# Optimization experiments

Measured on AMD Instinct MI355X. Metric: run time of the kernel, lower is better.

The kernel has to match this reference:

```python
import jax, jax.numpy as jnp
import numpy as np

# dims
B, T = 128, 1024
INP, HUMAN = 54, 64          # input_dim, output_dim (HUMAN_SIZE)
DEC, ENC = 256, 256          # decoder / encoder GRU sizes
K, H_PSI, LR_PSI = 16, 256, 32
N_PSI = DEC*DEC + DEC + DEC*INP + DEC*HUMAN + INP*(HUMAN-INP)  # 96540


def setup_inputs() -> dict:
    key = jax.random.key(0)
    ks = jax.random.split(key, 16)
    g = lambda i, shape, s=0.05: jax.random.normal(ks[i], shape, jnp.float32) * s
    return {
        "inputs": g(0, (B, T, INP), 1.0),
        "state": jnp.zeros((B, DEC), jnp.float32),
        "eps": g(1, (B, K), 1.0),
        # encoder GRUCell params (torch gate order r,z,n)
        "enc_Wih": g(2, (3*ENC, INP)),
        "enc_Whh": g(3, (3*ENC, ENC)),
        "enc_bih": jnp.zeros((3*ENC,), jnp.float32),
        "enc_bhh": jnp.zeros((3*ENC,), jnp.float32),
        # latent projections
        "to_mu": g(4, (K, ENC)),
        "to_lsigma": g(5, (K, ENC)),
        # psi hypernetwork MLP
        "W1": g(6, (H_PSI, K)),   "b1": jnp.zeros((H_PSI,), jnp.float32),
        "W2": g(7, (LR_PSI, H_PSI)), "b2": jnp.zeros((LR_PSI,), jnp.float32),
        "W3": g(8, (N_PSI, LR_PSI), 0.01), "b3": jnp.zeros((N_PSI,), jnp.float32),
        # shared decoder gate params (bias second half init to ones, as in module)
        "gru_Wih": g(9, (2*DEC, INP)),
        "gru_Whh": g(10, (DEC, 2*DEC)),
        "gru_bias": jnp.concatenate([jnp.zeros((DEC,)), jnp.ones((DEC,))]).astype(jnp.float32),
    }


def reference(inputs, state, eps, enc_Wih, enc_Whh, enc_bih, enc_bhh,
              to_mu, to_lsigma, W1, b1, W2, b2, W3, b3,
              gru_Wih, gru_Whh, gru_bias):
    x_tbd = jnp.swapaxes(inputs, 0, 1)  # [T,B,INP]

    # ---- encoder GRU scan (torch GRUCell semantics) ----
    def enc_step(h, x_t):
        gi = x_t @ enc_Wih.T + enc_bih
        gh = h @ enc_Whh.T + enc_bhh
        ir, iz, inn = jnp.split(gi, 3, axis=-1)
        hr, hz, hn = jnp.split(gh, 3, axis=-1)
        r = jax.nn.sigmoid(ir + hr)
        z = jax.nn.sigmoid(iz + hz)
        n = jnp.tanh(inn + r * hn)
        return (1 - z) * n + z * h, None

    h_enc, _ = jax.lax.scan(enc_step, jnp.zeros((inputs.shape[0], ENC), inputs.dtype), x_tbd)

    # ---- MT latent ----
    mu = h_enc @ to_mu.T                 # [B,K]
    logstd = h_enc @ to_lsigma.T         # [B,K]
    z_lat = mu + eps * jnp.exp(logstd)

    # ---- psi hypernetwork ----
    psi = jnp.tanh(z_lat @ W1.T + b1) @ W2.T + b2
    psi = psi @ W3.T + b3                # [B, N_PSI]

    o = 0
    Whh_p = psi[:, o:o+DEC*DEC].reshape(-1, DEC, DEC); o += DEC*DEC
    bh_p  = psi[:, o:o+DEC];                           o += DEC
    Wih_p = psi[:, o:o+DEC*INP].reshape(-1, DEC, INP); o += DEC*INP
    C_p   = psi[:, o:o+DEC*HUMAN].reshape(-1, DEC, HUMAN); o += DEC*HUMAN
    D_p   = psi[:, o:o+INP*(HUMAN-INP)].reshape(-1, INP, HUMAN-INP)

    # ---- per-sample hypernet-weighted GRU decoder, vectorized over batch ----
    def dec_step(h, x_t):  # h:[B,DEC], x_t:[B,INP]
        gx = x_t @ gru_Wih.T                       # [B,2*DEC]
        gh = h @ gru_Whh                           # [B,2*DEC]
        zt = jax.nn.sigmoid(gx[:, :DEC] + gh[:, :DEC] + gru_bias[:DEC])
        rt = jax.nn.sigmoid(gx[:, DEC:] + gh[:, DEC:] + gru_bias[DEC:])
        eta = jnp.tanh(jnp.einsum('bd,bhd->bh', x_t, Wih_p)
                       + rt * jnp.tanh(jnp.einsum('bh,bhg->bg', h, Whh_p) + bh_p))
        h_new = zt * h + (1 - zt) * eta
        return h_new, h_new

    h_last, dec_seq = jax.lax.scan(dec_step, state, x_tbd)
    dec_seq = jnp.swapaxes(dec_seq, 0, 1)          # [B,T,DEC]

    # yhat = dec@C + cat(zeros, x@D) ; residual adds inputs to first INP cols
    yD = jnp.einsum('btd,bde->bte', inputs, D_p)   # [B,T,HUMAN-INP]
    yhats = jnp.einsum('bth,bho->bto', dec_seq, C_p) + jnp.concatenate([inputs, yD], axis=-1)

    return yhats, mu, logstd, h_last
```

## Files before the change

kernel.cpp:

```cpp
#include <hip/hip_runtime.h>

#define BB 128
#define TT 1024
#define INP 54
#define HUM 64
#define NPSI 96540
#define OFF_BH 65536
#define OFF_WIH 65792
#define OFF_C 79616
#define OFF_D 96000
#define OUT_MU 8388608
#define OUT_LS 8390656
#define OUT_HL 8392704

typedef unsigned int u32;
typedef unsigned short u16;
typedef _Float16 h2 __attribute__((ext_vector_type(2)));

__device__ __forceinline__ u32 pk(float a, float b) {
    h2 v; v.x = (_Float16)a; v.y = (_Float16)b;
    return __builtin_bit_cast(u32, v);
}
__device__ __forceinline__ float f16tof(u16 v) {
    return (float)__builtin_bit_cast(_Float16, v);
}
__device__ __forceinline__ u16 ftof16(float v) {
    return __builtin_bit_cast(u16, (_Float16)v);
}
__device__ __forceinline__ float lo16f(u32 v) { return f16tof((u16)(v & 0xffffu)); }
__device__ __forceinline__ float hi16f(u32 v) { return f16tof((u16)(v >> 16)); }
__device__ __forceinline__ h2 bch2(u32 a) { return __builtin_bit_cast(h2, a); }
__device__ __forceinline__ float fd2(u32 a, u32 b, float c) {
#if __has_builtin(__builtin_amdgcn_fdot2)
    return __builtin_amdgcn_fdot2(bch2(a), bch2(b), c, false);
#else
    return c + lo16f(a) * lo16f(b) + hi16f(a) * hi16f(b);
#endif
}
__device__ __forceinline__ h2 pfma(u32 a, u32 b, h2 c) {
    return bch2(a) * bch2(b) + c;
}
__device__ __forceinline__ float h2tof(h2 s) { return (float)s.x + (float)s.y; }
__device__ __forceinline__ float fsig(float x) { return 1.f / (1.f + __expf(-x)); }
__device__ __forceinline__ float ftanh(float x) { float e = __expf(2.f * x); return 1.f - 2.f / (e + 1.f); }

__device__ __forceinline__ float qred(float v) {
#if __has_builtin(__builtin_amdgcn_mov_dpp)
    int x = __builtin_bit_cast(int, v);
    v += __builtin_bit_cast(float, __builtin_amdgcn_mov_dpp(x, 0xB1, 0xF, 0xF, true));
    x = __builtin_bit_cast(int, v);
    v += __builtin_bit_cast(float, __builtin_amdgcn_mov_dpp(x, 0x4E, 0xF, 0xF, true));
    return v;
#else
    v += __shfl_xor(v, 1); v += __shfl_xor(v, 2);
    return v;
#endif
}

__global__ __launch_bounds__(768, 3) void gemm_x_kernel(
    const float* __restrict__ inp, const float* __restrict__ W0,
    const u16* __restrict__ psi16, int mode, int t0, int len, int ct, int nt,
    u16* __restrict__ gout)
{
    const int tid = threadIdx.x;
    const int b = blockIdx.x / nt, tc = blockIdx.x % nt;
    const int gr = tid;
    float w[INP];
    if (mode == 0 || gr < 512) {
        const float* wsrc = W0 + (size_t)gr * INP;
#pragma unroll
        for (int c = 0; c < INP; ++c) w[c] = wsrc[c];
    } else {
        const u16* wsrc = psi16 + (size_t)b * NPSI + OFF_WIH + (size_t)(gr - 512) * INP;
#pragma unroll
        for (int c = 0; c < INP; ++c) w[c] = f16tof(wsrc[c]);
    }
    const int tb = tc * 128;
    const int te = (tb + 128 < len) ? tb + 128 : len;
    for (int tl = tb; tl < te; ++tl) {
        const float* xr = inp + ((size_t)b * TT + t0 + tl) * INP;
        float a = 0.f;
#pragma unroll
        for (int c = 0; c < INP; ++c) a = __builtin_fmaf(xr[c], w[c], a);
        gout[((size_t)b * ct + tl) * 768 + gr] = ftof16(a);
    }
}

__global__ __launch_bounds__(512) __attribute__((amdgpu_waves_per_eu(2, 2)))
void enc_scan_kernel(
    const u16* __restrict__ gi, int t0, int len, int ct,
    const float* __restrict__ Whh, const float* __restrict__ bih,
    const float* __restrict__ bhh, float* __restrict__ hcarry)
{
    __shared__ __align__(16) u32 hpp[2][144];
    __shared__ __align__(16) u32 gxs[2][3072];
    const int tid = threadIdx.x, b = blockIdx.x;
    const int l = tid & 3, g = tid >> 2;
    const int j0 = 2 * g, j1 = 2 * g + 1;

    u32 wr0[32], wz0[32], wn0[32], wr1[32], wz1[32], wn1[32];
    {
        const float* pr0 = Whh + (size_t)j0 * 256 + 64 * l;
        const float* pz0 = Whh + (size_t)(256 + j0) * 256 + 64 * l;
        const float* pn0 = Whh + (size_t)(512 + j0) * 256 + 64 * l;
        const float* pr1 = Whh + (size_t)j1 * 256 + 64 * l;
        const float* pz1 = Whh + (size_t)(256 + j1) * 256 + 64 * l;
        const float* pn1 = Whh + (size_t)(512 + j1) * 256 + 64 * l;
#pragma unroll
        for (int c = 0; c < 32; ++c) {
            wr0[c] = pk(pr0[2 * c], pr0[2 * c + 1]);
            wz0[c] = pk(pz0[2 * c], pz0[2 * c + 1]);
            wn0[c] = pk(pn0[2 * c], pn0[2 * c + 1]);
            wr1[c] = pk(pr1[2 * c], pr1[2 * c + 1]);
            wz1[c] = pk(pz1[2 * c], pz1[2 * c + 1]);
            wn1[c] = pk(pn1[2 * c], pn1[2 * c + 1]);
        }
    }
    const float brb0 = bih[j0] + bhh[j0],             brb1 = bih[j1] + bhh[j1];
    const float bzb0 = bih[256 + j0] + bhh[256 + j0], bzb1 = bih[256 + j1] + bhh[256 + j1];
    const float bib0 = bih[512 + j0],                 bib1 = bih[512 + j1];
    const float bhb0 = bhh[512 + j0],                 bhb1 = bhh[512 + j1];
    float hc0 = 0.f, hc1 = 0.f;
    if (t0 > 0) { hc0 = hcarry[(size_t)b * 256 + j0]; hc1 = hcarry[(size_t)b * 256 + j1]; }
    if (tid < 128) {
        u32 hv = 0u;
        if (t0 > 0) hv = pk(hcarry[(size_t)b * 256 + 2 * tid], hcarry[(size_t)b * 256 + 2 * tid + 1]);
        hpp[0][36 * (tid >> 5) + (tid & 31)] = hv;
    }
    const u32* gb32 = (const u32*)(gi + (size_t)b * ct * 768);
    {
        const int steps0 = (len < 8) ? len : 8;
#pragma unroll
        for (int k = 0; k < 6; ++k) {
            const int f = k * 512 + tid;
            if (f < 384 * steps0) gxs[0][f] = gb32[f];
        }
    }
    __syncthreads();

    const h2 z2 = {(_Float16)0.f, (_Float16)0.f};
    int buf = 0;
    for (int cb = 0; cb < len; cb += 8) {
        const int steps = (len - cb < 8) ? (len - cb) : 8;
        const int nsteps = (len - cb - 8 < 8) ? (len - cb - 8) : 8;
        u32 stg[6];
        if (nsteps > 0) {
            const u32* gsrc = gb32 + (size_t)(cb + 8) * 384;
#pragma unroll
            for (int k = 0; k < 6; ++k) {
                const int f = k * 512 + tid;
                if (f < 384 * nsteps) stg[k] = gsrc[f];
            }
        }
        for (int st = 0; st < steps; ++st) {
            const int tl = cb + st;
            const int p = tl & 1;
            const u32 c0 = gxs[buf][st * 384 + g];
            const u32 c1 = gxs[buf][st * 384 + 128 + g];
            const u32 c2 = gxs[buf][st * 384 + 256 + g];
            h2 vr0a = z2, vr0b = z2, vz0a = z2, vz0b = z2, vn0a = z2, vn0b = z2;
            h2 vr1a = z2, vr1b = z2, vz1a = z2, vz1b = z2, vn1a = z2, vn1b = z2;
            const uint4* hq = (const uint4*)hpp[p];
#pragma unroll
            for (int cc = 0; cc < 8; ++cc) {
                uint4 q = hq[9 * l + cc];
                u32 qa[4] = {q.x, q.y, q.z, q.w};
#pragma unroll
                for (int u = 0; u < 4; ++u) {
                    const int c = cc * 4 + u;
                    if (u & 1) {
                        vr0b = pfma(wr0[c], qa[u], vr0b);
                        vz0b = pfma(wz0[c], qa[u], vz0b);
                        vn0b = pfma(wn0[c], qa[u], vn0b);
                        vr1b = pfma(wr1[c], qa[u], vr1b);
                        vz1b = pfma(wz1[c], qa[u], vz1b);
                        vn1b = pfma(wn1[c], qa[u], vn1b);
                    } else {
                        vr0a = pfma(wr0[c], qa[u], vr0a);
                        vz0a = pfma(wz0[c], qa[u], vz0a);
                        vn0a = pfma(wn0[c], qa[u], vn0a);
                        vr1a = pfma(wr1[c], qa[u], vr1a);
                        vz1a = pfma(wz1[c], qa[u], vz1a);
                        vn1a = pfma(wn1[c], qa[u], vn1a);
                    }
                }
            }
            float ar0 = qred(h2tof(vr0a + vr0b));
            float az0 = qred(h2tof(vz0a + vz0b));
            float ah0 = qred(h2tof(vn0a + vn0b));
            float ar1 = qred(h2tof(vr1a + vr1b));
            float az1 = qred(h2tof(vz1a + vz1b));
            float ah1 = qred(h2tof(vn1a + vn1b));
            {
                float r0 = fsig(ar0 + lo16f(c0) + brb0);
                float z0 = fsig(az0 + lo16f(c1) + bzb0);
                float nn0 = ftanh(lo16f(c2) + bib0 + r0 * (ah0 + bhb0));
                float hn0 = (1.f - z0) * nn0 + z0 * hc0;
                float r1 = fsig(ar1 + hi16f(c0) + brb1);
                float z1 = fsig(az1 + hi16f(c1) + bzb1);
                float nn1 = ftanh(hi16f(c2) + bib1 + r1 * (ah1 + bhb1));
                float hn1 = (1.f - z1) * nn1 + z1 * hc1;
                hc0 = hn0; hc1 = hn1;
                if (l == 0) hpp[p ^ 1][36 * (g >> 5) + (g & 31)] = pk(hn0, hn1);
            }
            __syncthreads();
        }
        if (nsteps > 0) {
#pragma unroll
            for (int k = 0; k < 6; ++k) {
                const int f = k * 512 + tid;
                if (f < 384 * nsteps) gxs[buf ^ 1][f] = stg[k];
            }
        }
        __syncthreads();
        buf ^= 1;
    }
    if (l == 0) {
        hcarry[(size_t)b * 256 + j0] = hc0;
        hcarry[(size_t)b * 256 + j1] = hc1;
    }
}

__global__ __launch_bounds__(256) void latent_kernel(
    const float* __restrict__ henc, const float* __restrict__ eps,
    const float* __restrict__ to_mu, const float* __restrict__ to_ls,
    const float* __restrict__ W1, const float* __restrict__ b1,
    const float* __restrict__ W2, const float* __restrict__ b2,
    float* __restrict__ psi2, float* __restrict__ out)
{
    __shared__ float h[256], zz[16], p1[256];
    const int tid = threadIdx.x, b = blockIdx.x;
    h[tid] = henc[(size_t)b * 256 + tid];
    __syncthreads();
    if (tid < 16) {
        float m = 0, s = 0;
        for (int k = 0; k < 256; ++k) {
            m += h[k] * to_mu[tid * 256 + k];
            s += h[k] * to_ls[tid * 256 + k];
        }
        out[OUT_MU + b * 16 + tid] = m;
        out[OUT_LS + b * 16 + tid] = s;
        zz[tid] = m + eps[b * 16 + tid] * __expf(s);
    }
    __syncthreads();
    {
        float a = b1[tid];
        for (int k = 0; k < 16; ++k) a += zz[k] * W1[tid * 16 + k];
        p1[tid] = ftanh(a);
    }
    __syncthreads();
    if (tid < 32) {
        float a = b2[tid];
        for (int k = 0; k < 256; ++k) a += p1[k] * W2[tid * 256 + k];
        psi2[b * 32 + tid] = a;
    }
}

__global__ __launch_bounds__(256) void psi3_kernel(
    const float* __restrict__ psi2, const float* __restrict__ W3,
    const float* __restrict__ b3, u16* __restrict__ psi16)
{
    __shared__ float sp2[128 * 32];
    __shared__ float w3t[256 * 33];
    const int tid = threadIdx.x;
    const int n0 = blockIdx.x * 256;
    for (int idx = tid; idx < 4096; idx += 256) sp2[idx] = psi2[idx];
    for (int idx = tid; idx < 8192; idx += 256) {
        int row = idx >> 5, k = idx & 31;
        int n = n0 + row;
        w3t[row * 33 + k] = (n < NPSI) ? W3[(size_t)n * 32 + k] : 0.f;
    }
    __syncthreads();
    const int n = n0 + tid;
    if (n < NPSI) {
        float w[32];
#pragma unroll
        for (int k = 0; k < 32; ++k) w[k] = w3t[tid * 33 + k];
        const float bv = b3[n];
        for (int bi = 0; bi < 128; ++bi) {
            float a = bv;
#pragma unroll
            for (int k = 0; k < 32; ++k) a += sp2[bi * 32 + k] * w[k];
            psi16[(size_t)bi * NPSI + n] = ftof16(a);
        }
    }
}

__global__ __launch_bounds__(512) __attribute__((amdgpu_waves_per_eu(2, 2)))
void dec_scan_kernel(
    const u16* __restrict__ gx, int t0, int len, int ct,
    const float* __restrict__ state, const float* __restrict__ gWhh,
    const float* __restrict__ gbias, const u16* __restrict__ psi16,
    float* __restrict__ dcarry, u32* __restrict__ hseq, float* __restrict__ out)
{
    __shared__ __align__(16) u32 hpp[2][144];
    __shared__ __align__(16) u32 gxs[2][3072];
    const int tid = threadIdx.x, b = blockIdx.x;
    const int l = tid & 3, g = tid >> 2;
    const int j0 = 2 * g, j1 = 2 * g + 1;
    const u16* pc = psi16 + (size_t)b * NPSI;

    u32 wz0[32], wr0[32], wp0[32], wz1[32], wr1[32], wp1[32];
#pragma unroll
    for (int c = 0; c < 32; ++c) {
        const int h0 = 64 * l + 2 * c;
        wz0[c] = pk(gWhh[(size_t)h0 * 512 + j0], gWhh[(size_t)(h0 + 1) * 512 + j0]);
        wr0[c] = pk(gWhh[(size_t)h0 * 512 + 256 + j0], gWhh[(size_t)(h0 + 1) * 512 + 256 + j0]);
        wp0[c] = (u32)pc[(size_t)h0 * 256 + j0] | ((u32)pc[(size_t)(h0 + 1) * 256 + j0] << 16);
        wz1[c] = pk(gWhh[(size_t)h0 * 512 + j1], gWhh[(size_t)(h0 + 1) * 512 + j1]);
        wr1[c] = pk(gWhh[(size_t)h0 * 512 + 256 + j1], gWhh[(size_t)(h0 + 1) * 512 + 256 + j1]);
        wp1[c] = (u32)pc[(size_t)h0 * 256 + j1] | ((u32)pc[(size_t)(h0 + 1) * 256 + j1] << 16);
    }
    const float gzb0 = gbias[j0], gzb1 = gbias[j1];
    const float grb0 = gbias[256 + j0], grb1 = gbias[256 + j1];
    const float bhb0 = f16tof(pc[OFF_BH + j0]), bhb1 = f16tof(pc[OFF_BH + j1]);
    const float* hsrc = (t0 == 0) ? state : dcarry;
    float hc0 = hsrc[(size_t)b * 256 + j0];
    float hc1 = hsrc[(size_t)b * 256 + j1];
    if (tid < 128) hpp[0][36 * (tid >> 5) + (tid & 31)] =
        pk(hsrc[(size_t)b * 256 + 2 * tid], hsrc[(size_t)b * 256 + 2 * tid + 1]);
    const u32* gb32 = (const u32*)(gx + (size_t)b * ct * 768);
    {
        const int steps0 = (len < 8) ? len : 8;
#pragma unroll
        for (int k = 0; k < 6; ++k) {
            const int f = k * 512 + tid;
            if (f < 384 * steps0) gxs[0][f] = gb32[f];
        }
    }
    __syncthreads();

    u32* hsb = hseq + (size_t)b * TT * 128;
    int buf = 0;
    for (int cb = 0; cb < len; cb += 8) {
        const int steps = (len - cb < 8) ? (len - cb) : 8;
        const int nsteps = (len - cb - 8 < 8) ? (len - cb - 8) : 8;
        u32 stg[6];
        if (nsteps > 0) {
            const u32* gsrc = gb32 + (size_t)(cb + 8) * 384;
#pragma unroll
            for (int k = 0; k < 6; ++k) {
                const int f = k * 512 + tid;
                if (f < 384 * nsteps) stg[k] = gsrc[f];
            }
        }
        for (int st = 0; st < steps; ++st) {
            const int tl = cb + st;
            const int p = tl & 1;
            const u32 c0 = gxs[buf][st * 384 + g];
            const u32 c1 = gxs[buf][st * 384 + 128 + g];
            const u32 c2 = gxs[buf][st * 384 + 256 + g];
            float az0 = 0, ar0 = 0, ap0 = 0, az1 = 0, ar1 = 0, ap1 = 0;
            const uint4* hq = (const uint4*)hpp[p];
#pragma unroll
            for (int cc = 0; cc < 8; ++cc) {
                uint4 q = hq[9 * l + cc];
                u32 qa[4] = {q.x, q.y, q.z, q.w};
#pragma unroll
                for (int u = 0; u < 4; ++u) {
                    const int c = cc * 4 + u;
                    az0 = fd2(wz0[c], qa[u], az0);
                    ar0 = fd2(wr0[c], qa[u], ar0);
                    ap0 = fd2(wp0[c], qa[u], ap0);
                    az1 = fd2(wz1[c], qa[u], az1);
                    ar1 = fd2(wr1[c], qa[u], ar1);
                    ap1 = fd2(wp1[c], qa[u], ap1);
                }
            }
            az0 = qred(az0); ar0 = qred(ar0); ap0 = qred(ap0);
            az1 = qred(az1); ar1 = qred(ar1); ap1 = qred(ap1);
            {
                float zt0 = fsig(az0 + lo16f(c0) + gzb0);
                float rt0 = fsig(ar0 + lo16f(c1) + grb0);
                float eta0 = ftanh(lo16f(c2) + rt0 * ftanh(ap0 + bhb0));
                float hn0 = zt0 * hc0 + (1.f - zt0) * eta0;
                float zt1 = fsig(az1 + hi16f(c0) + gzb1);
                float rt1 = fsig(ar1 + hi16f(c1) + grb1);
                float eta1 = ftanh(hi16f(c2) + rt1 * ftanh(ap1 + bhb1));
                float hn1 = zt1 * hc1 + (1.f - zt1) * eta1;
                hc0 = hn0; hc1 = hn1;
                if (l == 0) {
                    u32 hv = pk(hn0, hn1);
                    hpp[p ^ 1][36 * (g >> 5) + (g & 31)] = hv;
                    hsb[(size_t)(t0 + tl) * 128 + g] = hv;
                }
            }
            __syncthreads();
        }
        if (nsteps > 0) {
#pragma unroll
            for (int k = 0; k < 6; ++k) {
                const int f = k * 512 + tid;
                if (f < 384 * nsteps) gxs[buf ^ 1][f] = stg[k];
            }
        }
        __syncthreads();
        buf ^= 1;
    }
    if (l == 0) {
        dcarry[(size_t)b * 256 + j0] = hc0;
        dcarry[(size_t)b * 256 + j1] = hc1;
        if (t0 + len == TT) {
            out[OUT_HL + (size_t)b * 256 + j0] = hc0;
            out[OUT_HL + (size_t)b * 256 + j1] = hc1;
        }
    }
}

#define YT 32
__global__ __launch_bounds__(256) void yhat_kernel(
    const u32* __restrict__ hseq, const u16* __restrict__ psi16,
    float* __restrict__ out)
{
    __shared__ float part[2][YT][64];
    const int tid = threadIdx.x;
    const int b = blockIdx.x >> 5, tile = blockIdx.x & 31;
    const int o = tid & 63, s = (tid >> 6) & 1, tq = tid >> 7;
    const u16* pc = psi16 + (size_t)b * NPSI;
    u32 cpr[64];
#pragma unroll
    for (int i = 0; i < 64; ++i) {
        const int gp = s * 64 + i;
        cpr[i] = (u32)pc[OFF_C + (size_t)(2 * gp) * 64 + o]
               | ((u32)pc[OFF_C + (size_t)(2 * gp + 1) * 64 + o] << 16);
    }
    const int t0 = tile * YT;
    for (int th = 0; th < YT / 2; ++th) {
        const int tl = tq * (YT / 2) + th;
        const uint4* h4 = (const uint4*)(hseq + ((size_t)b * TT + t0 + tl) * 128 + s * 64);
        float a = 0.f;
#pragma unroll
        for (int gc = 0; gc < 16; ++gc) {
            uint4 q = h4[gc];
            a = fd2(q.x, cpr[gc * 4 + 0], a);
            a = fd2(q.y, cpr[gc * 4 + 1], a);
            a = fd2(q.z, cpr[gc * 4 + 2], a);
            a = fd2(q.w, cpr[gc * 4 + 3], a);
        }
        part[s][tl][o] = a;
    }
    __syncthreads();
    for (int i = 0; i < 8; ++i) {
        const int flat = i * 256 + tid;
        const int tl = flat >> 6, o2 = flat & 63;
        out[((size_t)b * TT + t0 + tl) * HUM + o2] = part[0][tl][o2] + part[1][tl][o2];
    }
}

__global__ __launch_bounds__(256) void post_kernel(
    const float* __restrict__ inp, const u16* __restrict__ psi16,
    float* __restrict__ out)
{
    __shared__ float xs[128][55];
    __shared__ float ds[INP][10];
    const int tid = threadIdx.x;
    const int b = blockIdx.x >> 3, tile = blockIdx.x & 7;
    const int t0 = tile * 128;
    const u16* pc = psi16 + (size_t)b * NPSI;
    for (int idx = tid; idx < 540; idx += 256)
        ds[idx / 10][idx % 10] = f16tof(pc[OFF_D + idx]);
    for (int idx = tid; idx < 128 * INP; idx += 256) {
        const int t = idx / INP, d = idx % INP;
        xs[t][d] = inp[((size_t)b * TT + t0 + t) * INP + d];
    }
    __syncthreads();
    for (int i = 0; i < 32; ++i) {
        const int flat = i * 256 + tid;
        const int t = flat >> 6, o = flat & 63;
        const size_t oi = ((size_t)b * TT + t0 + t) * HUM + o;
        float y = out[oi];
        if (o < INP) y += xs[t][o];
        else {
            float acc = 0.f;
            for (int d = 0; d < INP; ++d) acc += xs[t][d] * ds[d][o - INP];
            y += acc;
        }
        out[oi] = y;
    }
}

extern "C" void kernel_launch(void* const* d_in, const int* in_sizes, int n_in,
                              void* d_out, int out_size, void* d_ws, size_t ws_size,
                              hipStream_t stream)
{
    const float* inputs = (const float*)d_in[0];
    const float* state  = (const float*)d_in[1];
    const float* eps    = (const float*)d_in[2];
    const float* eWih   = (const float*)d_in[3];
    const float* eWhh   = (const float*)d_in[4];
    const float* ebih   = (const float*)d_in[5];
    const float* ebhh   = (const float*)d_in[6];
    const float* to_mu  = (const float*)d_in[7];
    const float* to_ls  = (const float*)d_in[8];
    const float* W1     = (const float*)d_in[9];
    const float* b1     = (const float*)d_in[10];
    const float* W2     = (const float*)d_in[11];
    const float* b2     = (const float*)d_in[12];
    const float* W3     = (const float*)d_in[13];
    const float* b3     = (const float*)d_in[14];
    const float* gWih   = (const float*)d_in[15];
    const float* gWhh   = (const float*)d_in[16];
    const float* gbias  = (const float*)d_in[17];
    float* out = (float*)d_out;
    float* ws  = (float*)d_ws;

    float* henc   = ws;
    float* psi2   = ws + 32768;
    float* dcarry = ws + 36864;
    u16*   psi16  = (u16*)(ws + 69632);
    u32*   hseq   = (u32*)(ws + 6248192);
    u16*   gbuf   = (u16*)(ws + 23025408);
    const size_t used = (size_t)23025408 * 4;
    size_t avail = (ws_size > used + 4096) ? (ws_size - used - 4096) : 0;
    int ct = (int)(avail / ((size_t)BB * 768 * 2));
    if (ct > TT) ct = TT;
    if (ct < 1) ct = 1;

    for (int t0 = 0; t0 < TT; t0 += ct) {
        const int len = (TT - t0 < ct) ? (TT - t0) : ct;
        const int nt = (len + 127) / 128;
        gemm_x_kernel<<<BB * nt, 768, 0, stream>>>(inputs, eWih, psi16, 0, t0, len, ct, nt, gbuf);
        enc_scan_kernel<<<BB, 512, 0, stream>>>(gbuf, t0, len, ct, eWhh, ebih, ebhh, henc);
    }
    latent_kernel<<<BB, 256, 0, stream>>>(henc, eps, to_mu, to_ls, W1, b1, W2, b2, psi2, out);
    psi3_kernel<<<(NPSI + 255) / 256, 256, 0, stream>>>(psi2, W3, b3, psi16);
    for (int t0 = 0; t0 < TT; t0 += ct) {
        const int len = (TT - t0 < ct) ? (TT - t0) : ct;
        const int nt = (len + 127) / 128;
        gemm_x_kernel<<<BB * nt, 768, 0, stream>>>(inputs, gWih, psi16, 1, t0, len, ct, nt, gbuf);
        dec_scan_kernel<<<BB, 512, 0, stream>>>(gbuf, t0, len, ct, state, gWhh, gbias, psi16,
                                                dcarry, hseq, out);
    }
    yhat_kernel<<<BB * 32, 256, 0, stream>>>(hseq, psi16, out);
    post_kernel<<<BB * 8, 256, 0, stream>>>(inputs, psi16, out);
}
```

Before: 4.706 ms.

## Split scan kernels to one hidden unit per thread group with 1024 threads

```diff
diff --git a/kernel.cpp b/kernel.cpp
--- a/kernel.cpp
+++ b/kernel.cpp
@@ -37,10 +37,6 @@
     return c + lo16f(a) * lo16f(b) + hi16f(a) * hi16f(b);
 #endif
 }
-__device__ __forceinline__ h2 pfma(u32 a, u32 b, h2 c) {
-    return bch2(a) * bch2(b) + c;
-}
-__device__ __forceinline__ float h2tof(h2 s) { return (float)s.x + (float)s.y; }
 __device__ __forceinline__ float fsig(float x) { return 1.f / (1.f + __expf(-x)); }
 __device__ __forceinline__ float ftanh(float x) { float e = __expf(2.f * x); return 1.f - 2.f / (e + 1.f); }
 
@@ -86,42 +82,35 @@
     }
 }
 
-__global__ __launch_bounds__(512) __attribute__((amdgpu_waves_per_eu(2, 2)))
+__global__ __launch_bounds__(1024) __attribute__((amdgpu_waves_per_eu(4, 4)))
 void enc_scan_kernel(
     const u16* __restrict__ gi, int t0, int len, int ct,
     const float* __restrict__ Whh, const float* __restrict__ bih,
     const float* __restrict__ bhh, float* __restrict__ hcarry)
 {
     __shared__ __align__(16) u32 hpp[2][144];
-    __shared__ __align__(16) u32 gxs[2][3072];
+    __shared__ __align__(16) u32 gxs32[2][3072];
     const int tid = threadIdx.x, b = blockIdx.x;
     const int l = tid & 3, g = tid >> 2;
-    const int j0 = 2 * g, j1 = 2 * g + 1;
-
-    u32 wr0[32], wz0[32], wn0[32], wr1[32], wz1[32], wn1[32];
+
+    u32 wr[32], wz[32], wn[32];
     {
-        const float* pr0 = Whh + (size_t)j0 * 256 + 64 * l;
-        const float* pz0 = Whh + (size_t)(256 + j0) * 256 + 64 * l;
-        const float* pn0 = Whh + (size_t)(512 + j0) * 256 + 64 * l;
-        const float* pr1 = Whh + (size_t)j1 * 256 + 64 * l;
-        const float* pz1 = Whh + (size_t)(256 + j1) * 256 + 64 * l;
-        const float* pn1 = Whh + (size_t)(512 + j1) * 256 + 64 * l;
+        const float* pr = Whh + (size_t)g * 256 + 64 * l;
+        const float* pz = Whh + (size_t)(256 + g) * 256 + 64 * l;
+        const float* pn = Whh + (size_t)(512 + g) * 256 + 64 * l;
 #pragma unroll
         for (int c = 0; c < 32; ++c) {
-            wr0[c] = pk(pr0[2 * c], pr0[2 * c + 1]);
-            wz0[c] = pk(pz0[2 * c], pz0[2 * c + 1]);
-            wn0[c] = pk(pn0[2 * c], pn0[2 * c + 1]);
-            wr1[c] = pk(pr1[2 * c], pr1[2 * c + 1]);
-            wz1[c] = pk(pz1[2 * c], pz1[2 * c + 1]);
-            wn1[c] = pk(pn1[2 * c], pn1[2 * c + 1]);
-        }
-    }
-    const float brb0 = bih[j0] + bhh[j0],             brb1 = bih[j1] + bhh[j1];
-    const float bzb0 = bih[256 + j0] + bhh[256 + j0], bzb1 = bih[256 + j1] + bhh[256 + j1];
-    const float bib0 = bih[512 + j0],                 bib1 = bih[512 + j1];
-    const float bhb0 = bhh[512 + j0],                 bhb1 = bhh[512 + j1];
-    float hc0 = 0.f, hc1 = 0.f;
-    if (t0 > 0) { hc0 = hcarry[(size_t)b * 256 + j0]; hc1 = hcarry[(size_t)b * 256 + j1]; }
+            wr[c] = pk(pr[2 * c], pr[2 * c + 1]);
+            wz[c] = pk(pz[2 * c], pz[2 * c + 1]);
+            wn[c] = pk(pn[2 * c], pn[2 * c + 1]);
+        }
+    }
+    const float brb = bih[g] + bhh[g];
+    const float bzb = bih[256 + g] + bhh[256 + g];
+    const float bib = bih[512 + g];
+    const float bhb = bhh[512 + g];
+    float hc = 0.f;
+    if (t0 > 0) hc = hcarry[(size_t)b * 256 + g];
     if (tid < 128) {
         u32 hv = 0u;
         if (t0 > 0) hv = pk(hcarry[(size_t)b * 256 + 2 * tid], hcarry[(size_t)b * 256 + 2 * tid + 1]);
@@ -131,35 +120,30 @@
     {
         const int steps0 = (len < 8) ? len : 8;
 #pragma unroll
-        for (int k = 0; k < 6; ++k) {
-            const int f = k * 512 + tid;
-            if (f < 384 * steps0) gxs[0][f] = gb32[f];
-        }
-    }
-    __syncthreads();
-
-    const h2 z2 = {(_Float16)0.f, (_Float16)0.f};
+        for (int k = 0; k < 3; ++k) {
+            const int f = k * 1024 + tid;
+            if (f < 384 * steps0) gxs32[0][f] = gb32[f];
+        }
+    }
+    __syncthreads();
+
     int buf = 0;
     for (int cb = 0; cb < len; cb += 8) {
         const int steps = (len - cb < 8) ? (len - cb) : 8;
         const int nsteps = (len - cb - 8 < 8) ? (len - cb - 8) : 8;
-        u32 stg[6];
+        u32 stg[3];
         if (nsteps > 0) {
             const u32* gsrc = gb32 + (size_t)(cb + 8) * 384;
 #pragma unroll
-            for (int k = 0; k < 6; ++k) {
-                const int f = k * 512 + tid;
+            for (int k = 0; k < 3; ++k) {
+                const int f = k * 1024 + tid;
                 if (f < 384 * nsteps) stg[k] = gsrc[f];
             }
         }
         for (int st = 0; st < steps; ++st) {
             const int tl = cb + st;
             const int p = tl & 1;
-            const u32 c0 = gxs[buf][st * 384 + g];
-            const u32 c1 = gxs[buf][st * 384 + 128 + g];
-            const u32 c2 = gxs[buf][st * 384 + 256 + g];
-            h2 vr0a = z2, vr0b = z2, vz0a = z2, vz0b = z2, vn0a = z2, vn0b = z2;
-            h2 vr1a = z2, vr1b = z2, vz1a = z2, vz1b = z2, vn1a = z2, vn1b = z2;
+            float ar = 0, az = 0, ah = 0;
             const uint4* hq = (const uint4*)hpp[p];
 #pragma unroll
             for (int cc = 0; cc < 8; ++cc) {
@@ -168,57 +152,41 @@
 #pragma unroll
                 for (int u = 0; u < 4; ++u) {
                     const int c = cc * 4 + u;
-                    if (u & 1) {
-                        vr0b = pfma(wr0[c], qa[u], vr0b);
-                        vz0b = pfma(wz0[c], qa[u], vz0b);
-                        vn0b = pfma(wn0[c], qa[u], vn0b);
-                        vr1b = pfma(wr1[c], qa[u], vr1b);
-                        vz1b = pfma(wz1[c], qa[u], vz1b);
-                        vn1b = pfma(wn1[c], qa[u], vn1b);
-                    } else {
-                        vr0a = pfma(wr0[c], qa[u], vr0a);
-                        vz0a = pfma(wz0[c], qa[u], vz0a);
-                        vn0a = pfma(wn0[c], qa[u], vn0a);
-                        vr1a = pfma(wr1[c], qa[u], vr1a);
-                        vz1a = pfma(wz1[c], qa[u], vz1a);
-                        vn1a = pfma(wn1[c], qa[u], vn1a);
-                    }
+                    ar = fd2(wr[c], qa[u], ar);
+                    az = fd2(wz[c], qa[u], az);
+                    ah = fd2(wn[c], qa[u], ah);
                 }
             }
-            float ar0 = qred(h2tof(vr0a + vr0b));
-            float az0 = qred(h2tof(vz0a + vz0b));
-            float ah0 = qred(h2tof(vn0a + vn0b));
-            float ar1 = qred(h2tof(vr1a + vr1b));
-            float az1 = qred(h2tof(vz1a + vz1b));
-            float ah1 = qred(h2tof(vn1a + vn1b));
-            {
-                float r0 = fsig(ar0 + lo16f(c0) + brb0);
-                float z0 = fsig(az0 + lo16f(c1) + bzb0);
-                float nn0 = ftanh(lo16f(c2) + bib0 + r0 * (ah0 + bhb0));
-                float hn0 = (1.f - z0) * nn0 + z0 * hc0;
-                float r1 = fsig(ar1 + hi16f(c0) + brb1);
-                float z1 = fsig(az1 + hi16f(c1) + bzb1);
-                float nn1 = ftanh(hi16f(c2) + bib1 + r1 * (ah1 + bhb1));
-                float hn1 = (1.f - z1) * nn1 + z1 * hc1;
-                hc0 = hn0; hc1 = hn1;
-                if (l == 0) hpp[p ^ 1][36 * (g >> 5) + (g & 31)] = pk(hn0, hn1);
+            ar = qred(ar); az = qred(az); ah = qred(ah);
+            if (l == 0) {
+                const u16* gx16 = (const u16*)gxs32[buf];
+                const float c0 = f16tof(gx16[st * 768 + g]);
+                const float c1 = f16tof(gx16[st * 768 + 256 + g]);
+                const float c2 = f16tof(gx16[st * 768 + 512 + g]);
+                float r = fsig(ar + c0 + brb);
+                float z = fsig(az + c1 + bzb);
+                float nn = ftanh(c2 + bib + r * (ah + bhb));
+                float hn = (1.f - z) * nn + z * hc;
+                hc = hn;
+                float ho = __shfl_xor(hn, 4);
+                if (!(g & 1)) {
+                    const int gp = g >> 1;
+                    hpp[p ^ 1][36 * (gp >> 5) + (gp & 31)] = pk(hn, ho);
+                }
             }
             __syncthreads();
         }
         if (nsteps > 0) {
 #pragma unroll
-            for (int k = 0; k < 6; ++k) {
-                const int f = k * 512 + tid;
-                if (f < 384 * nsteps) gxs[buf ^ 1][f] = stg[k];
+            for (int k = 0; k < 3; ++k) {
+                const int f = k * 1024 + tid;
+                if (f < 384 * nsteps) gxs32[buf ^ 1][f] = stg[k];
             }
         }
         __syncthreads();
         buf ^= 1;
     }
-    if (l == 0) {
-        hcarry[(size_t)b * 256 + j0] = hc0;
-        hcarry[(size_t)b * 256 + j1] = hc1;
-    }
+    if (l == 0) hcarry[(size_t)b * 256 + g] = hc;
 }
 
 __global__ __launch_bounds__(256) void latent_kernel(
@@ -286,7 +254,7 @@
     }
 }
 
-__global__ __launch_bounds__(512) __attribute__((amdgpu_waves_per_eu(2, 2)))
+__global__ __launch_bounds__(1024) __attribute__((amdgpu_waves_per_eu(4, 4)))
 void dec_scan_kernel(
     const u16* __restrict__ gx, int t0, int len, int ct,
     const float* __restrict__ state, const float* __restrict__ gWhh,
@@ -294,38 +262,33 @@
     float* __restrict__ dcarry, u32* __restrict__ hseq, float* __restrict__ out)
 {
     __shared__ __align__(16) u32 hpp[2][144];
-    __shared__ __align__(16) u32 gxs[2][3072];
+    __shared__ __align__(16) u32 gxs32[2][3072];
     const int tid = threadIdx.x, b = blockIdx.x;
     const int l = tid & 3, g = tid >> 2;
-    const int j0 = 2 * g, j1 = 2 * g + 1;
     const u16* pc = psi16 + (size_t)b * NPSI;
 
-    u32 wz0[32], wr0[32], wp0[32], wz1[32], wr1[32], wp1[32];
+    u32 wz[32], wrr[32], wp[32];
 #pragma unroll
     for (int c = 0; c < 32; ++c) {
         const int h0 = 64 * l + 2 * c;
-        wz0[c] = pk(gWhh[(size_t)h0 * 512 + j0], gWhh[(size_t)(h0 + 1) * 512 + j0]);
-        wr0[c] = pk(gWhh[(size_t)h0 * 512 + 256 + j0], gWhh[(size_t)(h0 + 1) * 512 + 256 + j0]);
-        wp0[c] = (u32)pc[(size_t)h0 * 256 + j0] | ((u32)pc[(size_t)(h0 + 1) * 256 + j0] << 16);
-        wz1[c] = pk(gWhh[(size_t)h0 * 512 + j1], gWhh[(size_t)(h0 + 1) * 512 + j1]);
-        wr1[c] = pk(gWhh[(size_t)h0 * 512 + 256 + j1], gWhh[(size_t)(h0 + 1) * 512 + 256 + j1]);
-        wp1[c] = (u32)pc[(size_t)h0 * 256 + j1] | ((u32)pc[(size_t)(h0 + 1) * 256 + j1] << 16);
-    }
-    const float gzb0 = gbias[j0], gzb1 = gbias[j1];
-    const float grb0 = gbias[256 + j0], grb1 = gbias[256 + j1];
-    const float bhb0 = f16tof(pc[OFF_BH + j0]), bhb1 = f16tof(pc[OFF_BH + j1]);
+        wz[c]  = pk(gWhh[(size_t)h0 * 512 + g], gWhh[(size_t)(h0 + 1) * 512 + g]);
+        wrr[c] = pk(gWhh[(size_t)h0 * 512 + 256 + g], gWhh[(size_t)(h0 + 1) * 512 + 256 + g]);
+        wp[c]  = (u32)pc[(size_t)h0 * 256 + g] | ((u32)pc[(size_t)(h0 + 1) * 256 + g] << 16);
+    }
+    const float gzb = gbias[g];
+    const float grb = gbias[256 + g];
+    const float bhb = f16tof(pc[OFF_BH + g]);
     const float* hsrc = (t0 == 0) ? state : dcarry;
-    float hc0 = hsrc[(size_t)b * 256 + j0];
-    float hc1 = hsrc[(size_t)b * 256 + j1];
+    float hc = hsrc[(size_t)b * 256 + g];
     if (tid < 128) hpp[0][36 * (tid >> 5) + (tid & 31)] =
         pk(hsrc[(size_t)b * 256 + 2 * tid], hsrc[(size_t)b * 256 + 2 * tid + 1]);
     const u32* gb32 = (const u32*)(gx + (size_t)b * ct * 768);
     {
         const int steps0 = (len < 8) ? len : 8;
 #pragma unroll
-        for (int k = 0; k < 6; ++k) {
-            const int f = k * 512 + tid;
-            if (f < 384 * steps0) gxs[0][f] = gb32[f];
+        for (int k = 0; k < 3; ++k) {
+            const int f = k * 1024 + tid;
+            if (f < 384 * steps0) gxs32[0][f] = gb32[f];
         }
     }
     __syncthreads();
@@ -335,22 +298,19 @@
     for (int cb = 0; cb < len; cb += 8) {
         const int steps = (len - cb < 8) ? (len - cb) : 8;
         const int nsteps = (len - cb - 8 < 8) ? (len - cb - 8) : 8;
-        u32 stg[6];
+        u32 stg[3];
         if (nsteps > 0) {
             const u32* gsrc = gb32 + (size_t)(cb + 8) * 384;
 #pragma unroll
-            for (int k = 0; k < 6; ++k) {
-                const int f = k * 512 + tid;
+            for (int k = 0; k < 3; ++k) {
+                const int f = k * 1024 + tid;
                 if (f < 384 * nsteps) stg[k] = gsrc[f];
             }
         }
         for (int st = 0; st < steps; ++st) {
             const int tl = cb + st;
             const int p = tl & 1;
-            const u32 c0 = gxs[buf][st * 384 + g];
-            const u32 c1 = gxs[buf][st * 384 + 128 + g];
-            const u32 c2 = gxs[buf][st * 384 + 256 + g];
-            float az0 = 0, ar0 = 0, ap0 = 0, az1 = 0, ar1 = 0, ap1 = 0;
+            float az = 0, ar = 0, ap = 0;
             const uint4* hq = (const uint4*)hpp[p];
 #pragma unroll
             for (int cc = 0; cc < 8; ++cc) {
@@ -359,51 +319,45 @@
 #pragma unroll
                 for (int u = 0; u < 4; ++u) {
                     const int c = cc * 4 + u;
-                    az0 = fd2(wz0[c], qa[u], az0);
-                    ar0 = fd2(wr0[c], qa[u], ar0);
-                    ap0 = fd2(wp0[c], qa[u], ap0);
-                    az1 = fd2(wz1[c], qa[u], az1);
-                    ar1 = fd2(wr1[c], qa[u], ar1);
-                    ap1 = fd2(wp1[c], qa[u], ap1);
+                    az = fd2(wz[c], qa[u], az);
+                    ar = fd2(wrr[c], qa[u], ar);
+                    ap = fd2(wp[c], qa[u], ap);
                 }
             }
-            az0 = qred(az0); ar0 = qred(ar0); ap0 = qred(ap0);
-            az1 = qred(az1); ar1 = qred(ar1); ap1 = qred(ap1);
-            {
-                float zt0 = fsig(az0 + lo16f(c0) + gzb0);
-                float rt0 = fsig(ar0 + lo16f(c1) + grb0);
-                float eta0 = ftanh(lo16f(c2) + rt0 * ftanh(ap0 + bhb0));
-                float hn0 = zt0 * hc0 + (1.f - zt0) * eta0;
-                float zt1 = fsig(az1 + hi16f(c0) + gzb1);
-                float rt1 = fsig(ar1 + hi16f(c1) + grb1);
-                float eta1 = ftanh(hi16f(c2) + rt1 * ftanh(ap1 + bhb1));
-                float hn1 = zt1 * hc1 + (1.f - zt1) * eta1;
-                hc0 = hn0; hc1 = hn1;
-                if (l == 0) {
-                    u32 hv = pk(hn0, hn1);
-                    hpp[p ^ 1][36 * (g >> 5) + (g & 31)] = hv;
-                    hsb[(size_t)(t0 + tl) * 128 + g] = hv;
+            az = qred(az); ar = qred(ar); ap = qred(ap);
+            if (l == 0) {
+                const u16* gx16 = (const u16*)gxs32[buf];
+                const float c0 = f16tof(gx16[st * 768 + g]);
+                const float c1 = f16tof(gx16[st * 768 + 256 + g]);
+                const float c2 = f16tof(gx16[st * 768 + 512 + g]);
+                float zt = fsig(az + c0 + gzb);
+                float rt = fsig(ar + c1 + grb);
+                float eta = ftanh(c2 + rt * ftanh(ap + bhb));
+                float hn = zt * hc + (1.f - zt) * eta;
+                hc = hn;
+                float ho = __shfl_xor(hn, 4);
+                if (!(g & 1)) {
+                    const int gp = g >> 1;
+                    u32 hv = pk(hn, ho);
+                    hpp[p ^ 1][36 * (gp >> 5) + (gp & 31)] = hv;
+                    hsb[(size_t)(t0 + tl) * 128 + gp] = hv;
                 }
             }
             __syncthreads();
         }
         if (nsteps > 0) {
 #pragma unroll
-            for (int k = 0; k < 6; ++k) {
-                const int f = k * 512 + tid;
-                if (f < 384 * nsteps) gxs[buf ^ 1][f] = stg[k];
+            for (int k = 0; k < 3; ++k) {
+                const int f = k * 1024 + tid;
+                if (f < 384 * nsteps) gxs32[buf ^ 1][f] = stg[k];
             }
         }
         __syncthreads();
         buf ^= 1;
     }
     if (l == 0) {
-        dcarry[(size_t)b * 256 + j0] = hc0;
-        dcarry[(size_t)b * 256 + j1] = hc1;
-        if (t0 + len == TT) {
-            out[OUT_HL + (size_t)b * 256 + j0] = hc0;
-            out[OUT_HL + (size_t)b * 256 + j1] = hc1;
-        }
+        dcarry[(size_t)b * 256 + g] = hc;
+        if (t0 + len == TT) out[OUT_HL + (size_t)b * 256 + g] = hc;
     }
 }
 
@@ -520,7 +474,7 @@
         const int len = (TT - t0 < ct) ? (TT - t0) : ct;
         const int nt = (len + 127) / 128;
         gemm_x_kernel<<<BB * nt, 768, 0, stream>>>(inputs, eWih, psi16, 0, t0, len, ct, nt, gbuf);
-        enc_scan_kernel<<<BB, 512, 0, stream>>>(gbuf, t0, len, ct, eWhh, ebih, ebhh, henc);
+        enc_scan_kernel<<<BB, 1024, 0, stream>>>(gbuf, t0, len, ct, eWhh, ebih, ebhh, henc);
     }
     latent_kernel<<<BB, 256, 0, stream>>>(henc, eps, to_mu, to_ls, W1, b1, W2, b2, psi2, out);
     psi3_kernel<<<(NPSI + 255) / 256, 256, 0, stream>>>(psi2, W3, b3, psi16);
@@ -528,8 +482,8 @@
         const int len = (TT - t0 < ct) ? (TT - t0) : ct;
         const int nt = (len + 127) / 128;
         gemm_x_kernel<<<BB * nt, 768, 0, stream>>>(inputs, gWih, psi16, 1, t0, len, ct, nt, gbuf);
-        dec_scan_kernel<<<BB, 512, 0, stream>>>(gbuf, t0, len, ct, state, gWhh, gbias, psi16,
-                                                dcarry, hseq, out);
+        dec_scan_kernel<<<BB, 1024, 0, stream>>>(gbuf, t0, len, ct, state, gWhh, gbias, psi16,
+                                                 dcarry, hseq, out);
     }
     yhat_kernel<<<BB * 32, 256, 0, stream>>>(hseq, psi16, out);
     post_kernel<<<BB * 8, 256, 0, stream>>>(inputs, psi16, out);
```

After: 5.173 ms. 1.1x slower.

## Simplify encoder scan: per-step register prefetch of gates and fp32 dot2 accumulation

Applied to the files above, without the earlier changes.

```diff
diff --git a/kernel.cpp b/kernel.cpp
--- a/kernel.cpp
+++ b/kernel.cpp
@@ -37,10 +37,6 @@
     return c + lo16f(a) * lo16f(b) + hi16f(a) * hi16f(b);
 #endif
 }
-__device__ __forceinline__ h2 pfma(u32 a, u32 b, h2 c) {
-    return bch2(a) * bch2(b) + c;
-}
-__device__ __forceinline__ float h2tof(h2 s) { return (float)s.x + (float)s.y; }
 __device__ __forceinline__ float fsig(float x) { return 1.f / (1.f + __expf(-x)); }
 __device__ __forceinline__ float ftanh(float x) { float e = __expf(2.f * x); return 1.f - 2.f / (e + 1.f); }
 
@@ -93,7 +89,6 @@
     const float* __restrict__ bhh, float* __restrict__ hcarry)
 {
     __shared__ __align__(16) u32 hpp[2][144];
-    __shared__ __align__(16) u32 gxs[2][3072];
     const int tid = threadIdx.x, b = blockIdx.x;
     const int l = tid & 3, g = tid >> 2;
     const int j0 = 2 * g, j1 = 2 * g + 1;
@@ -127,93 +122,55 @@
         if (t0 > 0) hv = pk(hcarry[(size_t)b * 256 + 2 * tid], hcarry[(size_t)b * 256 + 2 * tid + 1]);
         hpp[0][36 * (tid >> 5) + (tid & 31)] = hv;
     }
-    const u32* gb32 = (const u32*)(gi + (size_t)b * ct * 768);
-    {
-        const int steps0 = (len < 8) ? len : 8;
-#pragma unroll
-        for (int k = 0; k < 6; ++k) {
-            const int f = k * 512 + tid;
-            if (f < 384 * steps0) gxs[0][f] = gb32[f];
-        }
-    }
-    __syncthreads();
-
-    const h2 z2 = {(_Float16)0.f, (_Float16)0.f};
-    int buf = 0;
-    for (int cb = 0; cb < len; cb += 8) {
-        const int steps = (len - cb < 8) ? (len - cb) : 8;
-        const int nsteps = (len - cb - 8 < 8) ? (len - cb - 8) : 8;
-        u32 stg[6];
-        if (nsteps > 0) {
-            const u32* gsrc = gb32 + (size_t)(cb + 8) * 384;
-#pragma unroll
-            for (int k = 0; k < 6; ++k) {
-                const int f = k * 512 + tid;
-                if (f < 384 * nsteps) stg[k] = gsrc[f];
+    __syncthreads();
+
+    const u16* gbase = gi + (size_t)b * ct * 768;
+    u32 c0 = *(const u32*)(gbase + 2 * g);
+    u32 c1 = *(const u32*)(gbase + 256 + 2 * g);
+    u32 c2 = *(const u32*)(gbase + 512 + 2 * g);
+
+    for (int tl = 0; tl < len; ++tl) {
+        const int p = tl & 1;
+        u32 n0 = 0, n1 = 0, n2 = 0;
+        if (tl + 1 < len) {
+            const u16* gn = gbase + (size_t)(tl + 1) * 768;
+            n0 = *(const u32*)(gn + 2 * g);
+            n1 = *(const u32*)(gn + 256 + 2 * g);
+            n2 = *(const u32*)(gn + 512 + 2 * g);
+        }
+        float ar0 = 0, az0 = 0, ah0 = 0, ar1 = 0, az1 = 0, ah1 = 0;
+        const uint4* hq = (const uint4*)hpp[p];
+#pragma unroll
+        for (int cc = 0; cc < 8; ++cc) {
+            uint4 q = hq[9 * l + cc];
+            u32 qa[4] = {q.x, q.y, q.z, q.w};
+#pragma unroll
+            for (int u = 0; u < 4; ++u) {
+                const int c = cc * 4 + u;
+                ar0 = fd2(wr0[c], qa[u], ar0);
+                az0 = fd2(wz0[c], qa[u], az0);
+                ah0 = fd2(wn0[c], qa[u], ah0);
+                ar1 = fd2(wr1[c], qa[u], ar1);
+                az1 = fd2(wz1[c], qa[u], az1);
+                ah1 = fd2(wn1[c], qa[u], ah1);
             }
         }
-        for (int st = 0; st < steps; ++st) {
-            const int tl = cb + st;
-            const int p = tl & 1;
-            const u32 c0 = gxs[buf][st * 384 + g];
-            const u32 c1 = gxs[buf][st * 384 + 128 + g];
-            const u32 c2 = gxs[buf][st * 384 + 256 + g];
-            h2 vr0a = z2, vr0b = z2, vz0a = z2, vz0b = z2, vn0a = z2, vn0b = z2;
-            h2 vr1a = z2, vr1b = z2, vz1a = z2, vz1b = z2, vn1a = z2, vn1b = z2;
-            const uint4* hq = (const uint4*)hpp[p];
-#pragma unroll
-            for (int cc = 0; cc < 8; ++cc) {
-                uint4 q = hq[9 * l + cc];
-                u32 qa[4] = {q.x, q.y, q.z, q.w};
-#pragma unroll
-                for (int u = 0; u < 4; ++u) {
-                    const int c = cc * 4 + u;
-                    if (u & 1) {
-                        vr0b = pfma(wr0[c], qa[u], vr0b);
-                        vz0b = pfma(wz0[c], qa[u], vz0b);
-                        vn0b = pfma(wn0[c], qa[u], vn0b);
-                        vr1b = pfma(wr1[c], qa[u], vr1b);
-                        vz1b = pfma(wz1[c], qa[u], vz1b);
-                        vn1b = pfma(wn1[c], qa[u], vn1b);
-                    } else {
-                        vr0a = pfma(wr0[c], qa[u], vr0a);
-                        vz0a = pfma(wz0[c], qa[u], vz0a);
-                        vn0a = pfma(wn0[c], qa[u], vn0a);
-                        vr1a = pfma(wr1[c], qa[u], vr1a);
-                        vz1a = pfma(wz1[c], qa[u], vz1a);
-                        vn1a = pfma(wn1[c], qa[u], vn1a);
-                    }
-                }
-            }
-            float ar0 = qred(h2tof(vr0a + vr0b));
-            float az0 = qred(h2tof(vz0a + vz0b));
-            float ah0 = qred(h2tof(vn0a + vn0b));
-            float ar1 = qred(h2tof(vr1a + vr1b));
-            float az1 = qred(h2tof(vz1a + vz1b));
-            float ah1 = qred(h2tof(vn1a + vn1b));
-            {
-                float r0 = fsig(ar0 + lo16f(c0) + brb0);
-                float z0 = fsig(az0 + lo16f(c1) + bzb0);
-                float nn0 = ftanh(lo16f(c2) + bib0 + r0 * (ah0 + bhb0));
-                float hn0 = (1.f - z0) * nn0 + z0 * hc0;
-                float r1 = fsig(ar1 + hi16f(c0) + brb1);
-                float z1 = fsig(az1 + hi16f(c1) + bzb1);
-                float nn1 = ftanh(hi16f(c2) + bib1 + r1 * (ah1 + bhb1));
-                float hn1 = (1.f - z1) * nn1 + z1 * hc1;
-                hc0 = hn0; hc1 = hn1;
-                if (l == 0) hpp[p ^ 1][36 * (g >> 5) + (g & 31)] = pk(hn0, hn1);
-            }
-            __syncthreads();
-        }
-        if (nsteps > 0) {
-#pragma unroll
-            for (int k = 0; k < 6; ++k) {
-                const int f = k * 512 + tid;
-                if (f < 384 * nsteps) gxs[buf ^ 1][f] = stg[k];
-            }
-        }
+        ar0 = qred(ar0); az0 = qred(az0); ah0 = qred(ah0);
+        ar1 = qred(ar1); az1 = qred(az1); ah1 = qred(ah1);
+        {
+            float r0 = fsig(ar0 + lo16f(c0) + brb0);
+            float z0 = fsig(az0 + lo16f(c1) + bzb0);
+            float nn0 = ftanh(lo16f(c2) + bib0 + r0 * (ah0 + bhb0));
+            float hn0 = (1.f - z0) * nn0 + z0 * hc0;
+            float r1 = fsig(ar1 + hi16f(c0) + brb1);
+            float z1 = fsig(az1 + hi16f(c1) + bzb1);
+            float nn1 = ftanh(hi16f(c2) + bib1 + r1 * (ah1 + bhb1));
+            float hn1 = (1.f - z1) * nn1 + z1 * hc1;
+            hc0 = hn0; hc1 = hn1;
+            if (l == 0) hpp[p ^ 1][36 * (g >> 5) + (g & 31)] = pk(hn0, hn1);
+        }
+        c0 = n0; c1 = n1; c2 = n2;
         __syncthreads();
-        buf ^= 1;
     }
     if (l == 0) {
         hcarry[(size_t)b * 256 + j0] = hc0;
@@ -294,7 +251,7 @@
     float* __restrict__ dcarry, u32* __restrict__ hseq, float* __restrict__ out)
 {
     __shared__ __align__(16) u32 hpp[2][144];
-    __shared__ __align__(16) u32 gxs[2][3072];
+    __shared__ __align__(16) u32 gxs32[2][3072];
     const int tid = threadIdx.x, b = blockIdx.x;
     const int l = tid & 3, g = tid >> 2;
     const int j0 = 2 * g, j1 = 2 * g + 1;
@@ -325,7 +282,7 @@
 #pragma unroll
         for (int k = 0; k < 6; ++k) {
             const int f = k * 512 + tid;
-            if (f < 384 * steps0) gxs[0][f] = gb32[f];
+            if (f < 384 * steps0) gxs32[0][f] = gb32[f];
         }
     }
     __syncthreads();
@@ -347,9 +304,10 @@
         for (int st = 0; st < steps; ++st) {
             const int tl = cb + st;
             const int p = tl & 1;
-            const u32 c0 = gxs[buf][st * 384 + g];
-            const u32 c1 = gxs[buf][st * 384 + 128 + g];
-            const u32 c2 = gxs[buf][st * 384 + 256 + g];
+            const u16* gx16 = (const u16*)gxs32[buf];
+            const u32 c0 = *(const u32*)(gx16 + st * 768 + 2 * g);
+            const u32 c1 = *(const u32*)(gx16 + st * 768 + 256 + 2 * g);
+            const u32 c2 = *(const u32*)(gx16 + st * 768 + 512 + 2 * g);
             float az0 = 0, ar0 = 0, ap0 = 0, az1 = 0, ar1 = 0, ap1 = 0;
             const uint4* hq = (const uint4*)hpp[p];
 #pragma unroll
@@ -391,7 +349,7 @@
 #pragma unroll
             for (int k = 0; k < 6; ++k) {
                 const int f = k * 512 + tid;
-                if (f < 384 * nsteps) gxs[buf ^ 1][f] = stg[k];
+                if (f < 384 * nsteps) gxs32[buf ^ 1][f] = stg[k];
             }
         }
         __syncthreads();
```

Result: faster. 4.531 ms (-3.7%).
